# Performance work log

Measured on AMD Instinct MI355X. Metric: run time of the kernel, lower is better.

The kernel has to match this reference:

```python
import jax, jax.numpy as jnp
import numpy as np

E = 256      # feat_dim
H = 4        # num_heads
D = E // H   # head_dim = 64
NC = 7       # num_classes
B = 65536
EPS = 1e-5


def layernorm(x, g, b):
    mu = jnp.mean(x, axis=-1, keepdims=True)
    var = jnp.mean((x - mu) ** 2, axis=-1, keepdims=True)
    return (x - mu) * jax.lax.rsqrt(var + EPS) * g + b


def setup_inputs() -> dict:
    key = jax.random.key(0)
    ks = jax.random.split(key, 16)
    s = 0.02
    return {
        "f_swin":   jax.random.normal(ks[0], (B, E), jnp.float32),
        "f_maxvit": jax.random.normal(ks[1], (B, E), jnp.float32),
        "f_focal":  jax.random.normal(ks[2], (B, E), jnp.float32),
        # MultiheadAttention params (torch packs q,k,v into in_proj)
        "in_proj_w": jax.random.normal(ks[3], (3 * E, E), jnp.float32) * s,
        "in_proj_b": jnp.zeros((3 * E,), jnp.float32),
        "out_w": jax.random.normal(ks[4], (E, E), jnp.float32) * s,
        "out_b": jnp.zeros((E,), jnp.float32),
        # fusion LayerNorm
        "ln1_g": jnp.ones((E,), jnp.float32),
        "ln1_b": jnp.zeros((E,), jnp.float32),
        # gate: Linear(3E, 3)
        "gate_w": jax.random.normal(ks[5], (3, 3 * E), jnp.float32) * s,
        "gate_b": jnp.zeros((3,), jnp.float32),
        # deep_head: LN -> Linear(E,256) -> GELU -> Linear(256,128) -> GELU -> Linear(128,7)
        "ln2_g": jnp.ones((E,), jnp.float32),
        "ln2_b": jnp.zeros((E,), jnp.float32),
        "w1": jax.random.normal(ks[6], (256, E), jnp.float32) * s,
        "b1": jnp.zeros((256,), jnp.float32),
        "w2": jax.random.normal(ks[7], (128, 256), jnp.float32) * s,
        "b2": jnp.zeros((128,), jnp.float32),
        "w3": jax.random.normal(ks[8], (NC, 128), jnp.float32) * s,
        "b3": jnp.zeros((NC,), jnp.float32),
    }


def reference(f_swin, f_maxvit, f_focal, in_proj_w, in_proj_b, out_w, out_b,
              ln1_g, ln1_b, gate_w, gate_b, ln2_g, ln2_b,
              w1, b1, w2, b2, w3, b3):
    # --- AttentionFusionModule ---
    stacked = jnp.stack([f_swin, f_maxvit, f_focal], axis=1)  # [B,3,E]
    qkv = stacked @ in_proj_w.T + in_proj_b                   # [B,3,3E]
    q, k, v = jnp.split(qkv, 3, axis=-1)
    # [B,3,E] -> [B,H,3,D]
    def to_heads(t):
        return t.reshape(t.shape[0], 3, H, D).transpose(0, 2, 1, 3)
    qh, kh, vh = to_heads(q), to_heads(k), to_heads(v)
    scores = jnp.einsum('bhqd,bhkd->bhqk', qh, kh) / jnp.sqrt(jnp.float32(D))
    attn = jax.nn.softmax(scores, axis=-1)
    ctx = jnp.einsum('bhqk,bhkd->bhqd', attn, vh)             # [B,H,3,D]
    ctx = ctx.transpose(0, 2, 1, 3).reshape(-1, 3, E)         # [B,3,E]
    att_out = ctx @ out_w.T + out_b
    x = layernorm(att_out + stacked, ln1_g, ln1_b)            # [B,3,E]
    concat = jnp.concatenate([f_swin, f_maxvit, f_focal], axis=-1)  # [B,3E]
    weights = jax.nn.softmax(concat @ gate_w.T + gate_b, axis=-1)   # [B,3]
    fused = jnp.einsum('bse,bs->be', x, weights)              # [B,E]
    # --- deep_head (Dropout inactive at inference; exact GELU as in torch) ---
    h = layernorm(fused, ln2_g, ln2_b)
    h = jax.nn.gelu(h @ w1.T + b1, approximate=False)
    h = jax.nn.gelu(h @ w2.T + b2, approximate=False)
    logits = h @ w3.T + b3
    return logits, fused
```

## Files before the change

kernel.cpp:

```cpp
#include <hip/hip_runtime.h>
#include <math.h>


#define E   256
#define NC  7
#define BM  16
#define TOK 48
#define NT  256
#define BSX 264
#define BSB 136

typedef unsigned short u16;
typedef unsigned int   u32;
typedef __attribute__((ext_vector_type(8))) short  short8;
typedef __attribute__((ext_vector_type(4))) float  f32x4;

#define O_IPW 0
#define O_OW  196608
#define O_GW  262144
#define O_W1  264448
#define O_W2  329984
#define CVT_TOTAL 362752

__device__ __forceinline__ float bf2f(u32 u) { return __uint_as_float(u << 16); }
__device__ __forceinline__ u16 f2bf(float f) {
    u32 u = __float_as_uint(f);
    return (u16)((u + 0x7fffu + ((u >> 16) & 1u)) >> 16);
}

__global__ void cvt_weights(const float* __restrict__ ipw, const float* __restrict__ ow,
                            const float* __restrict__ gw,  const float* __restrict__ w1,
                            const float* __restrict__ w2,  u16* __restrict__ ws) {
    int i4 = (blockIdx.x * 256 + threadIdx.x) * 4;
    if (i4 >= CVT_TOTAL) return;
    const float* src; int off;
    if      (i4 < O_OW)  { src = ipw; off = i4; }
    else if (i4 < O_GW)  { src = ow;  off = i4 - O_OW; }
    else if (i4 < O_W1)  { src = gw;  off = i4 - O_GW; }
    else if (i4 < O_W2)  { src = w1;  off = i4 - O_W1; }
    else                 { src = w2;  off = i4 - O_W2; }
    float4 v = *(const float4*)(src + off);
    ushort4 o;
    o.x = f2bf(v.x); o.y = f2bf(v.y); o.z = f2bf(v.z); o.w = f2bf(v.w);
    *(ushort4*)(ws + i4) = o;
}

template<int MT, int NTW, int KSN, int AS, bool ZERO>
__device__ __forceinline__ void gemm_tile(const u16* aLds, int aRow0, int aCol0,
                                          const u16* __restrict__ bW, int rowBase, int bCol0,
                                          int lane, f32x4 (&acc)[MT][NTW]) {
    const int l16 = lane & 15, quad = lane >> 4;
    if (ZERO) {
        #pragma unroll
        for (int m = 0; m < MT; ++m)
            #pragma unroll
            for (int j = 0; j < NTW; ++j) acc[m][j] = (f32x4){0.f, 0.f, 0.f, 0.f};
    }
    #pragma unroll
    for (int ks = 0; ks < KSN; ++ks) {
        short8 a[MT];
        #pragma unroll
        for (int m = 0; m < MT; ++m)
            a[m] = *(const short8*)(aLds + (size_t)(aRow0 + m * 16 + l16) * AS + aCol0 + ks * 32 + quad * 8);
        #pragma unroll
        for (int j = 0; j < NTW; ++j) {
            short8 b = *(const short8*)(bW + (size_t)(rowBase + j * 16 + l16) * 256 + bCol0 + ks * 32 + quad * 8);
            #pragma unroll
            for (int m = 0; m < MT; ++m)
                acc[m][j] = __builtin_amdgcn_mfma_f32_16x16x32_bf16(a[m], b, acc[m][j], 0, 0, 0);
        }
    }
}

__global__ __launch_bounds__(NT, 2)
void dhc_mfma_kernel(
    const float* __restrict__ f0, const float* __restrict__ f1, const float* __restrict__ f2,
    const float* __restrict__ ipb, const float* __restrict__ ob,
    const float* __restrict__ ln1g, const float* __restrict__ ln1b,
    const float* __restrict__ gb,
    const float* __restrict__ ln2g, const float* __restrict__ ln2b,
    const float* __restrict__ b1, const float* __restrict__ b2,
    const float* __restrict__ w3, const float* __restrict__ b3,
    const u16* __restrict__ ws, float* __restrict__ d_out, int nrows)
{
    __shared__ __align__(16) u16 s_x[TOK * BSX];
    __shared__ __align__(16) u16 s_buf[TOK * BSB];
    __shared__ __align__(16) float s_small[640];
    #define S_ATTN(r,h,q) s_small[((r) * 4 + (h)) * 9 + (q)]

    const int tid  = threadIdx.x;
    const int wid  = tid >> 6, lane = tid & 63;
    const int l16  = lane & 15, quad = lane >> 4;
    const long long row0 = (long long)blockIdx.x * BM;
    const size_t fused_base = (size_t)nrows * NC;

    auto gp_slot = [&](int i) -> float* {
        return (float*)(s_x + (i >> 2) * BSX + 256) + (i & 3);
    };

    const u16* ipw_b = ws + O_IPW;
    const u16* ow_b  = ws + O_OW;
    const u16* gw_b  = ws + O_GW;
    const u16* w1_b  = ws + O_W1;
    const u16* w2_b  = ws + O_W2;

    #pragma unroll
    for (int it = 0; it < 12; ++it) {
        int id = it * NT + tid;
        int t  = id >> 6;
        int c4 = (id & 63) * 4;
        int s  = t >> 4, r = t & 15;
        float4 v = {0.f, 0.f, 0.f, 0.f};
        if (row0 + r < nrows) {
            const float* src = (s == 0 ? f0 : (s == 1 ? f1 : f2));
            v = *(const float4*)(src + (size_t)(row0 + r) * E + c4);
        }
        ushort4 o;
        o.x = f2bf(v.x); o.y = f2bf(v.y); o.z = f2bf(v.z); o.w = f2bf(v.w);
        *(ushort4*)(s_x + t * BSX + c4) = o;
    }
    __syncthreads();

    auto softmax_head = [&](int hh) {
        int i = tid >> 4, r = tid & 15;
        const u16* qrow = s_buf + (i * 16 + r) * BSB;
        const u16* k0 = s_buf + (0 * 16 + r) * BSB + 64;
        const u16* k1 = s_buf + (1 * 16 + r) * BSB + 64;
        const u16* k2 = s_buf + (2 * 16 + r) * BSB + 64;
        float d0a = 0.f, d0b = 0.f, d1a = 0.f, d1b = 0.f, d2a = 0.f, d2b = 0.f;
        #pragma unroll
        for (int d8 = 0; d8 < 8; ++d8) {
            short8 qv = *(const short8*)(qrow + d8 * 8);
            short8 a0 = *(const short8*)(k0 + d8 * 8);
            short8 a1 = *(const short8*)(k1 + d8 * 8);
            short8 a2 = *(const short8*)(k2 + d8 * 8);
            #pragma unroll
            for (int e = 0; e < 4; ++e) {
                float qa = bf2f((u32)(u16)qv[e]);
                float qb = bf2f((u32)(u16)qv[e + 4]);
                d0a += qa * bf2f((u32)(u16)a0[e]); d0b += qb * bf2f((u32)(u16)a0[e + 4]);
                d1a += qa * bf2f((u32)(u16)a1[e]); d1b += qb * bf2f((u32)(u16)a1[e + 4]);
                d2a += qa * bf2f((u32)(u16)a2[e]); d2b += qb * bf2f((u32)(u16)a2[e + 4]);
            }
        }
        float d0 = (d0a + d0b) * 0.125f, d1 = (d1a + d1b) * 0.125f, d2 = (d2a + d2b) * 0.125f;
        float mx = fmaxf(d0, fmaxf(d1, d2));
        float e0 = __expf(d0 - mx), e1 = __expf(d1 - mx), e2 = __expf(d2 - mx);
        float inv = 1.f / (e0 + e1 + e2);
        S_ATTN(r, hh, i * 3 + 0) = e0 * inv;
        S_ATTN(r, hh, i * 3 + 1) = e1 * inv;
        S_ATTN(r, hh, i * 3 + 2) = e2 * inv;
    };

    for (int h = 0; h < 4; ++h) {
        const int rbh = (wid < 2) ? (64 * h + 32 * wid)
                                  : (256 + 64 * h + 32 * (wid - 2));
        f32x4 acc[3][2];
        gemm_tile<3, 2, 8, BSX, true>(s_x, 0, 0, ipw_b, rbh, 0, lane, acc);
        if (h > 0 && tid < 48) softmax_head(h - 1);
        if (h == 0 && tid >= 48 && tid < 192) {
            int idx = tid - 48;
            int r = idx / 9, rem = idx % 9;
            int g = rem / 3, s = rem % 3;
            const u16* xp = s_x + (s * 16 + r) * BSX;
            const u16* wp = gw_b + g * 768 + s * 256;
            float a0 = 0.f, a1 = 0.f, a2 = 0.f, a3 = 0.f;
            for (int c8 = 0; c8 < 8; ++c8) {
                #pragma unroll
                for (int q4 = 0; q4 < 4; ++q4) {
                    short8 xv = *(const short8*)(xp + (c8 * 4 + q4) * 8);
                    short8 wv = *(const short8*)(wp + (c8 * 4 + q4) * 8);
                    float t = 0.f;
                    #pragma unroll
                    for (int e = 0; e < 8; ++e)
                        t += bf2f((u32)(u16)xv[e]) * bf2f((u32)(u16)wv[e]);
                    if      (q4 == 0) a0 += t;
                    else if (q4 == 1) a1 += t;
                    else if (q4 == 2) a2 += t;
                    else              a3 += t;
                }
            }
            *gp_slot(idx) = (a0 + a1) + (a2 + a3);
        }
        if (h == 1 && tid >= 48 && tid < 64) {
            int r = tid - 48;
            float l[3];
            #pragma unroll
            for (int g = 0; g < 3; ++g)
                l[g] = gb[g] + *gp_slot(r * 9 + g * 3 + 0)
                             + *gp_slot(r * 9 + g * 3 + 1)
                             + *gp_slot(r * 9 + g * 3 + 2);
            float mx = fmaxf(l[0], fmaxf(l[1], l[2]));
            float e0 = __expf(l[0] - mx), e1 = __expf(l[1] - mx), e2 = __expf(l[2] - mx);
            float inv = 1.f / (e0 + e1 + e2);
            s_small[576 + r * 3 + 0] = e0 * inv;
            s_small[576 + r * 3 + 1] = e1 * inv;
            s_small[576 + r * 3 + 2] = e2 * inv;
        }
        __syncthreads();
        const int nl = (wid < 2) ? (32 * wid) : (64 + 32 * (wid - 2));
        #pragma unroll
        for (int j = 0; j < 2; ++j) {
            int nn = nl + j * 16 + l16;
            float bias = ipb[rbh + j * 16 + l16];
            #pragma unroll
            for (int m = 0; m < 3; ++m)
                #pragma unroll
                for (int rr = 0; rr < 4; ++rr) {
                    int tok = m * 16 + quad * 4 + rr;
                    s_buf[tok * BSB + nn] = f2bf(acc[m][j][rr] + bias);
                }
        }
        __syncthreads();
    }

    f32x4 acc3[3][4];

    for (int hv = 0; hv < 2; ++hv) {
        {
            const int rb = 512 + 128 * hv + 32 * wid;
            f32x4 acc[3][2];
            gemm_tile<3, 2, 8, BSX, true>(s_x, 0, 0, ipw_b, rb, 0, lane, acc);
            if (hv == 0 && tid < 48) softmax_head(3);
            __syncthreads();
            #pragma unroll
            for (int j = 0; j < 2; ++j) {
                int nn = 32 * wid + j * 16 + l16;
                float bias = ipb[rb + j * 16 + l16];
                #pragma unroll
                for (int m = 0; m < 3; ++m)
                    #pragma unroll
                    for (int rr = 0; rr < 4; ++rr) {
                        int tok = m * 16 + quad * 4 + rr;
                        s_buf[tok * BSB + nn] = f2bf(acc[m][j][rr] + bias);
                    }
            }
        }
        __syncthreads();
        {
            int r  = tid >> 4;
            int cb = (tid & 15) * 8;
            int h  = 2 * hv + (cb >> 6);
            float a[9];
            #pragma unroll
            for (int q2 = 0; q2 < 9; ++q2) a[q2] = S_ATTN(r, h, q2);
            #pragma unroll
            for (int cc = 0; cc < 8; ++cc) {
                int c = cb + cc;
                float v0 = bf2f((u32)s_buf[(0 * 16 + r) * BSB + c]);
                float v1 = bf2f((u32)s_buf[(1 * 16 + r) * BSB + c]);
                float v2 = bf2f((u32)s_buf[(2 * 16 + r) * BSB + c]);
                float c0 = a[0] * v0 + a[1] * v1 + a[2] * v2;
                float c1 = a[3] * v0 + a[4] * v1 + a[5] * v2;
                float c2 = a[6] * v0 + a[7] * v1 + a[8] * v2;
                s_buf[(0 * 16 + r) * BSB + c] = f2bf(c0);
                s_buf[(1 * 16 + r) * BSB + c] = f2bf(c1);
                s_buf[(2 * 16 + r) * BSB + c] = f2bf(c2);
            }
        }
        __syncthreads();
        if (hv == 0) {
            gemm_tile<3, 4, 4, BSB, true >(s_buf, 0, 0, ow_b, 64 * wid, 0,   lane, acc3);
        } else {
            gemm_tile<3, 4, 4, BSB, false>(s_buf, 0, 0, ow_b, 64 * wid, 128, lane, acc3);
            #pragma unroll
            for (int j = 0; j < 4; ++j) {
                int n = 64 * wid + j * 16 + l16;
                float bias = ob[n];
                #pragma unroll
                for (int m = 0; m < 3; ++m)
                    #pragma unroll
                    for (int rr = 0; rr < 4; ++rr) {
                        int tok = m * 16 + quad * 4 + rr;
                        float v = acc3[m][j][rr] + bias + bf2f((u32)s_x[tok * BSX + n]);
                        s_x[tok * BSX + n] = f2bf(v);
                    }
            }
        }
        __syncthreads();
    }

    if (tid < 192) {
        int r = tid >> 2, j = tid & 3;
        const u16* xp = s_x + r * BSX + j * 64;
        float s0 = 0.f, s1 = 0.f, q0 = 0.f, q1 = 0.f;
        #pragma unroll
        for (int c8 = 0; c8 < 8; ++c8) {
            short8 v = *(const short8*)(xp + c8 * 8);
            #pragma unroll
            for (int e = 0; e < 4; ++e) {
                float xa = bf2f((u32)(u16)v[e]);
                float xb = bf2f((u32)(u16)v[e + 4]);
                s0 += xa; q0 += xa * xa;
                s1 += xb; q1 += xb * xb;
            }
        }
        float sum = s0 + s1, sq = q0 + q1;
        sum += __shfl_xor(sum, 1); sq += __shfl_xor(sq, 1);
        sum += __shfl_xor(sum, 2); sq += __shfl_xor(sq, 2);
        if (j == 0) {
            float mu = sum * (1.f / 256.f);
            float var = sq * (1.f / 256.f) - mu * mu;
            s_small[r] = mu;
            s_small[48 + r] = rsqrtf(var + 1e-5f);
        }
    }
    __syncthreads();
    {
        float g = ln1g[tid], b = ln1b[tid];
        #pragma unroll 4
        for (int t = 0; t < TOK; ++t) {
            float x = bf2f((u32)s_x[t * BSX + tid]);
            s_x[t * BSX + tid] = f2bf((x - s_small[t]) * s_small[48 + t] * g + b);
        }
    }
    __syncthreads();

    {
        int c = tid;
        float* outF = d_out + fused_base;
        #pragma unroll 4
        for (int r = 0; r < BM; ++r) {
            float w0 = s_small[576 + r * 3 + 0];
            float w1v = s_small[576 + r * 3 + 1];
            float w2v = s_small[576 + r * 3 + 2];
            float f = w0  * bf2f((u32)s_x[(0 * 16 + r) * BSX + c])
                    + w1v * bf2f((u32)s_x[(1 * 16 + r) * BSX + c])
                    + w2v * bf2f((u32)s_x[(2 * 16 + r) * BSX + c]);
            if (row0 + r < nrows) outF[(size_t)(row0 + r) * E + c] = f;
            s_buf[r * BSX + c] = f2bf(f);
        }
    }
    __syncthreads();

    {
        int r = tid >> 4, j = tid & 15;
        const u16* fp = s_buf + r * BSX + j * 16;
        float sum = 0.f, sq = 0.f;
        #pragma unroll
        for (int c8 = 0; c8 < 2; ++c8) {
            short8 v = *(const short8*)(fp + c8 * 8);
            #pragma unroll
            for (int e = 0; e < 8; ++e) {
                float x = bf2f((u32)(u16)v[e]);
                sum += x; sq += x * x;
            }
        }
        sum += __shfl_xor(sum, 1); sq += __shfl_xor(sq, 1);
        sum += __shfl_xor(sum, 2); sq += __shfl_xor(sq, 2);
        sum += __shfl_xor(sum, 4); sq += __shfl_xor(sq, 4);
        sum += __shfl_xor(sum, 8); sq += __shfl_xor(sq, 8);
        if (j == 0) {
            float mu = sum * (1.f / 256.f);
            float var = sq * (1.f / 256.f) - mu * mu;
            s_small[96 + r] = mu;
            s_small[112 + r] = rsqrtf(var + 1e-5f);
        }
    }
    __syncthreads();
    {
        float g = ln2g[tid], b = ln2b[tid];
        #pragma unroll
        for (int r = 0; r < BM; ++r) {
            float x = bf2f((u32)s_buf[r * BSX + tid]);
            s_buf[r * BSX + tid] = f2bf((x - s_small[96 + r]) * s_small[112 + r] * g + b);
        }
    }
    __syncthreads();

    {
        f32x4 acc[1][4];
        gemm_tile<1, 4, 8, BSX, true>(s_buf, 0, 0, w1_b, 64 * wid, 0, lane, acc);
        __syncthreads();
        #pragma unroll
        for (int j = 0; j < 4; ++j) {
            int n = 64 * wid + j * 16 + l16;
            float bias = b1[n];
            #pragma unroll
            for (int rr = 0; rr < 4; ++rr) {
                int r = quad * 4 + rr;
                float x = acc[0][j][rr] + bias;
                float hgelu = 0.5f * x * (1.f + erff(x * 0.70710678118654752f));
                s_buf[r * BSX + n] = f2bf(hgelu);
            }
        }
    }
    __syncthreads();

    {
        f32x4 acc[1][2];
        gemm_tile<1, 2, 8, BSX, true>(s_buf, 0, 0, w2_b, 32 * wid, 0, lane, acc);
        __syncthreads();
        #pragma unroll
        for (int j = 0; j < 2; ++j) {
            int n = 32 * wid + j * 16 + l16;
            float bias = b2[n];
            #pragma unroll
            for (int rr = 0; rr < 4; ++rr) {
                int r = quad * 4 + rr;
                float x = acc[0][j][rr] + bias;
                float hgelu = 0.5f * x * (1.f + erff(x * 0.70710678118654752f));
                s_buf[r * BSB + n] = f2bf(hgelu);
            }
        }
    }
    __syncthreads();

    if (tid < BM * NC) {
        int r = tid / NC, n = tid % NC;
        const float* wr = w3 + n * 128;
        const u16* hp = s_buf + r * BSB;
        float a0 = 0.f, a1 = 0.f, a2 = 0.f, a3 = 0.f;
        #pragma unroll
        for (int q8 = 0; q8 < 8; ++q8) {
            #pragma unroll
            for (int q4 = 0; q4 < 4; ++q4) {
                int k4 = q8 * 4 + q4;
                float4 w = *(const float4*)(wr + k4 * 4);
                float t = bf2f((u32)hp[k4 * 4 + 0]) * w.x
                        + bf2f((u32)hp[k4 * 4 + 1]) * w.y
                        + bf2f((u32)hp[k4 * 4 + 2]) * w.z
                        + bf2f((u32)hp[k4 * 4 + 3]) * w.w;
                if      (q4 == 0) a0 += t;
                else if (q4 == 1) a1 += t;
                else if (q4 == 2) a2 += t;
                else              a3 += t;
            }
        }
        float acc = b3[n] + (a0 + a1) + (a2 + a3);
        if (row0 + r < nrows) d_out[(size_t)(row0 + r) * NC + n] = acc;
    }
}

extern "C" void kernel_launch(void* const* d_in, const int* in_sizes, int n_in,
                              void* d_out, int out_size, void* d_ws, size_t ws_size,
                              hipStream_t stream) {
    (void)n_in; (void)ws_size; (void)out_size;
    const int nrows = in_sizes[0] / E;
    u16* ws = (u16*)d_ws;
    cvt_weights<<<(CVT_TOTAL / 4 + 255) / 256, 256, 0, stream>>>(
        (const float*)d_in[3], (const float*)d_in[5], (const float*)d_in[9],
        (const float*)d_in[13], (const float*)d_in[15], ws);
    const int nblocks = (nrows + BM - 1) / BM;
    dhc_mfma_kernel<<<nblocks, NT, 0, stream>>>(
        (const float*)d_in[0], (const float*)d_in[1], (const float*)d_in[2],
        (const float*)d_in[4], (const float*)d_in[6],
        (const float*)d_in[7], (const float*)d_in[8],
        (const float*)d_in[10],
        (const float*)d_in[11], (const float*)d_in[12],
        (const float*)d_in[14], (const float*)d_in[16],
        (const float*)d_in[17], (const float*)d_in[18],
        ws, (float*)d_out, nrows);
}
```

Measured before the change: 716.5 us.

## Make each wave process its own rows independently, eliminating block barriers

Restructures the kernel so each of the four waves owns four batch rows (twelve tokens) with private LDS slices, removing all __syncthreads between stages. GEMMs become single-16-row-tile MFMA loops over full weight width per wave, with token tiles padded to sixteen. This removes barrier stalls and cross-wave coordination but wastes MFMA rows on padding and multiplies per-row weight reads from global/L2.

```diff
diff --git a/kernel.cpp b/kernel.cpp
--- a/kernel.cpp
+++ b/kernel.cpp
@@ -5,7 +5,6 @@
 #define E   256
 #define NC  7
 #define BM  16
-#define TOK 48
 #define NT  256
 #define BSX 264
 #define BSB 136
@@ -45,29 +44,22 @@
     *(ushort4*)(ws + i4) = o;
 }
 
-template<int MT, int NTW, int KSN, int AS, bool ZERO>
-__device__ __forceinline__ void gemm_tile(const u16* aLds, int aRow0, int aCol0,
-                                          const u16* __restrict__ bW, int rowBase, int bCol0,
-                                          int lane, f32x4 (&acc)[MT][NTW]) {
+template<int NTW, int KSN, bool ZERO>
+__device__ __forceinline__ void gemm1(const u16* aBase, int aStride, 
+                                      const u16* __restrict__ bW, int rowBase, int bCol0,
+                                      int lane, f32x4 (&acc)[NTW]) {
     const int l16 = lane & 15, quad = lane >> 4;
     if (ZERO) {
         #pragma unroll
-        for (int m = 0; m < MT; ++m)
-            #pragma unroll
-            for (int j = 0; j < NTW; ++j) acc[m][j] = (f32x4){0.f, 0.f, 0.f, 0.f};
+        for (int j = 0; j < NTW; ++j) acc[j] = (f32x4){0.f, 0.f, 0.f, 0.f};
     }
     #pragma unroll
     for (int ks = 0; ks < KSN; ++ks) {
-        short8 a[MT];
-        #pragma unroll
-        for (int m = 0; m < MT; ++m)
-            a[m] = *(const short8*)(aLds + (size_t)(aRow0 + m * 16 + l16) * AS + aCol0 + ks * 32 + quad * 8);
+        short8 a = *(const short8*)(aBase + (size_t)l16 * aStride + ks * 32 + quad * 8);
         #pragma unroll
         for (int j = 0; j < NTW; ++j) {
             short8 b = *(const short8*)(bW + (size_t)(rowBase + j * 16 + l16) * 256 + bCol0 + ks * 32 + quad * 8);
-            #pragma unroll
-            for (int m = 0; m < MT; ++m)
-                acc[m][j] = __builtin_amdgcn_mfma_f32_16x16x32_bf16(a[m], b, acc[m][j], 0, 0, 0);
+            acc[j] = __builtin_amdgcn_mfma_f32_16x16x32_bf16(a, b, acc[j], 0, 0, 0);
         }
     }
 }
@@ -83,20 +75,19 @@
     const float* __restrict__ w3, const float* __restrict__ b3,
     const u16* __restrict__ ws, float* __restrict__ d_out, int nrows)
 {
-    __shared__ __align__(16) u16 s_x[TOK * BSX];
-    __shared__ __align__(16) u16 s_buf[TOK * BSB];
-    __shared__ __align__(16) float s_small[640];
-    #define S_ATTN(r,h,q) s_small[((r) * 4 + (h)) * 9 + (q)]
+    __shared__ __align__(16) u16 s_x[64 * BSX];
+    __shared__ __align__(16) u16 s_buf[64 * BSB];
+    __shared__ __align__(16) float s_small[4 * 192];
 
     const int tid  = threadIdx.x;
     const int wid  = tid >> 6, lane = tid & 63;
     const int l16  = lane & 15, quad = lane >> 4;
-    const long long row0 = (long long)blockIdx.x * BM;
+    const long long row0 = (long long)blockIdx.x * BM + wid * 4;
     const size_t fused_base = (size_t)nrows * NC;
 
-    auto gp_slot = [&](int i) -> float* {
-        return (float*)(s_x + (i >> 2) * BSX + 256) + (i & 3);
-    };
+    u16*   sx = s_x   + wid * 16 * BSX;
+    u16*   sb = s_buf + wid * 16 * BSB;
+    float* sm = s_small + wid * 192;
 
     const u16* ipw_b = ws + O_IPW;
     const u16* ow_b  = ws + O_OW;
@@ -105,184 +96,158 @@
     const u16* w2_b  = ws + O_W2;
 
     #pragma unroll
-    for (int it = 0; it < 12; ++it) {
-        int id = it * NT + tid;
-        int t  = id >> 6;
-        int c4 = (id & 63) * 4;
-        int s  = t >> 4, r = t & 15;
+    for (int t = 0; t < 12; ++t) {
+        int s = t >> 2, r = t & 3;
         float4 v = {0.f, 0.f, 0.f, 0.f};
         if (row0 + r < nrows) {
             const float* src = (s == 0 ? f0 : (s == 1 ? f1 : f2));
-            v = *(const float4*)(src + (size_t)(row0 + r) * E + c4);
+            v = *(const float4*)(src + (size_t)(row0 + r) * E + lane * 4);
         }
         ushort4 o;
         o.x = f2bf(v.x); o.y = f2bf(v.y); o.z = f2bf(v.z); o.w = f2bf(v.w);
-        *(ushort4*)(s_x + t * BSX + c4) = o;
-    }
-    __syncthreads();
-
-    auto softmax_head = [&](int hh) {
-        int i = tid >> 4, r = tid & 15;
-        const u16* qrow = s_buf + (i * 16 + r) * BSB;
-        const u16* k0 = s_buf + (0 * 16 + r) * BSB + 64;
-        const u16* k1 = s_buf + (1 * 16 + r) * BSB + 64;
-        const u16* k2 = s_buf + (2 * 16 + r) * BSB + 64;
-        float d0a = 0.f, d0b = 0.f, d1a = 0.f, d1b = 0.f, d2a = 0.f, d2b = 0.f;
-        #pragma unroll
-        for (int d8 = 0; d8 < 8; ++d8) {
-            short8 qv = *(const short8*)(qrow + d8 * 8);
-            short8 a0 = *(const short8*)(k0 + d8 * 8);
-            short8 a1 = *(const short8*)(k1 + d8 * 8);
-            short8 a2 = *(const short8*)(k2 + d8 * 8);
-            #pragma unroll
-            for (int e = 0; e < 4; ++e) {
-                float qa = bf2f((u32)(u16)qv[e]);
-                float qb = bf2f((u32)(u16)qv[e + 4]);
-                d0a += qa * bf2f((u32)(u16)a0[e]); d0b += qb * bf2f((u32)(u16)a0[e + 4]);
-                d1a += qa * bf2f((u32)(u16)a1[e]); d1b += qb * bf2f((u32)(u16)a1[e + 4]);
-                d2a += qa * bf2f((u32)(u16)a2[e]); d2b += qb * bf2f((u32)(u16)a2[e + 4]);
-            }
-        }
-        float d0 = (d0a + d0b) * 0.125f, d1 = (d1a + d1b) * 0.125f, d2 = (d2a + d2b) * 0.125f;
-        float mx = fmaxf(d0, fmaxf(d1, d2));
-        float e0 = __expf(d0 - mx), e1 = __expf(d1 - mx), e2 = __expf(d2 - mx);
-        float inv = 1.f / (e0 + e1 + e2);
-        S_ATTN(r, hh, i * 3 + 0) = e0 * inv;
-        S_ATTN(r, hh, i * 3 + 1) = e1 * inv;
-        S_ATTN(r, hh, i * 3 + 2) = e2 * inv;
-    };
+        *(ushort4*)(sx + t * BSX + lane * 4) = o;
+    }
+    {
+        ushort4 z = {0, 0, 0, 0};
+        #pragma unroll
+        for (int t = 12; t < 16; ++t) *(ushort4*)(sx + t * BSX + lane * 4) = z;
+    }
+
+    if (lane < 36) {
+        int r = lane / 9, rem = lane % 9, g = rem / 3, s = rem % 3;
+        const u16* xp = sx + (s * 4 + r) * BSX;
+        const u16* wp = gw_b + g * 768 + s * 256;
+        float a0 = 0.f, a1 = 0.f, a2 = 0.f, a3 = 0.f;
+        #pragma unroll
+        for (int c8 = 0; c8 < 8; ++c8) {
+            #pragma unroll
+            for (int q4 = 0; q4 < 4; ++q4) {
+                short8 xv = *(const short8*)(xp + (c8 * 4 + q4) * 8);
+                short8 wv = *(const short8*)(wp + (c8 * 4 + q4) * 8);
+                float t = 0.f;
+                #pragma unroll
+                for (int e = 0; e < 8; ++e)
+                    t += bf2f((u32)(u16)xv[e]) * bf2f((u32)(u16)wv[e]);
+                if      (q4 == 0) a0 += t;
+                else if (q4 == 1) a1 += t;
+                else if (q4 == 2) a2 += t;
+                else              a3 += t;
+            }
+        }
+        float part = (a0 + a1) + (a2 + a3);
+        int base = r * 9 + g * 3;
+        float tot = __shfl(part, base) + __shfl(part, base + 1) + __shfl(part, base + 2);
+        float logit = tot + gb[g];
+        int br = r * 9;
+        float l0 = __shfl(logit, br + 0);
+        float l1 = __shfl(logit, br + 3);
+        float l2 = __shfl(logit, br + 6);
+        float mx = fmaxf(l0, fmaxf(l1, l2));
+        float e0 = __expf(l0 - mx), e1 = __expf(l1 - mx), e2 = __expf(l2 - mx);
+        float w = __expf(logit - mx) / (e0 + e1 + e2);
+        if (s == 0) sm[144 + r * 3 + g] = w;
+    }
 
     for (int h = 0; h < 4; ++h) {
-        const int rbh = (wid < 2) ? (64 * h + 32 * wid)
-                                  : (256 + 64 * h + 32 * (wid - 2));
-        f32x4 acc[3][2];
-        gemm_tile<3, 2, 8, BSX, true>(s_x, 0, 0, ipw_b, rbh, 0, lane, acc);
-        if (h > 0 && tid < 48) softmax_head(h - 1);
-        if (h == 0 && tid >= 48 && tid < 192) {
-            int idx = tid - 48;
-            int r = idx / 9, rem = idx % 9;
-            int g = rem / 3, s = rem % 3;
-            const u16* xp = s_x + (s * 16 + r) * BSX;
-            const u16* wp = gw_b + g * 768 + s * 256;
-            float a0 = 0.f, a1 = 0.f, a2 = 0.f, a3 = 0.f;
-            for (int c8 = 0; c8 < 8; ++c8) {
+        f32x4 aq[4], ak[4];
+        gemm1<4, 8, true>(sx, BSX, ipw_b, 64 * h, 0, lane, aq);
+        gemm1<4, 8, true>(sx, BSX, ipw_b, 256 + 64 * h, 0, lane, ak);
+        #pragma unroll
+        for (int j = 0; j < 4; ++j) {
+            float bq_ = ipb[64 * h + j * 16 + l16];
+            float bk_ = ipb[256 + 64 * h + j * 16 + l16];
+            #pragma unroll
+            for (int rr = 0; rr < 4; ++rr) {
+                int tok = quad * 4 + rr;
+                sb[tok * BSB + j * 16 + l16]      = f2bf(aq[j][rr] + bq_);
+                sb[tok * BSB + 64 + j * 16 + l16] = f2bf(ak[j][rr] + bk_);
+            }
+        }
+        if (lane < 12) {
+            int r = lane / 3, i = lane % 3;
+            const u16* qrow = sb + (i * 4 + r) * BSB;
+            const u16* k0 = sb + (0 + r) * BSB + 64;
+            const u16* k1 = sb + (4 + r) * BSB + 64;
+            const u16* k2 = sb + (8 + r) * BSB + 64;
+            float d0a = 0.f, d0b = 0.f, d1a = 0.f, d1b = 0.f, d2a = 0.f, d2b = 0.f;
+            #pragma unroll
+            for (int d8 = 0; d8 < 8; ++d8) {
+                short8 qv = *(const short8*)(qrow + d8 * 8);
+                short8 a0 = *(const short8*)(k0 + d8 * 8);
+                short8 a1 = *(const short8*)(k1 + d8 * 8);
+                short8 a2 = *(const short8*)(k2 + d8 * 8);
                 #pragma unroll
-                for (int q4 = 0; q4 < 4; ++q4) {
-                    short8 xv = *(const short8*)(xp + (c8 * 4 + q4) * 8);
-                    short8 wv = *(const short8*)(wp + (c8 * 4 + q4) * 8);
-                    float t = 0.f;
-                    #pragma unroll
-                    for (int e = 0; e < 8; ++e)
-                        t += bf2f((u32)(u16)xv[e]) * bf2f((u32)(u16)wv[e]);
-                    if      (q4 == 0) a0 += t;
-                    else if (q4 == 1) a1 += t;
-                    else if (q4 == 2) a2 += t;
-                    else              a3 += t;
+                for (int e = 0; e < 4; ++e) {
+                    float qa = bf2f((u32)(u16)qv[e]);
+                    float qb = bf2f((u32)(u16)qv[e + 4]);
+                    d0a += qa * bf2f((u32)(u16)a0[e]); d0b += qb * bf2f((u32)(u16)a0[e + 4]);
+                    d1a += qa * bf2f((u32)(u16)a1[e]); d1b += qb * bf2f((u32)(u16)a1[e + 4]);
+                    d2a += qa * bf2f((u32)(u16)a2[e]); d2b += qb * bf2f((u32)(u16)a2[e + 4]);
                 }
             }
-            *gp_slot(idx) = (a0 + a1) + (a2 + a3);
-        }
-        if (h == 1 && tid >= 48 && tid < 64) {
-            int r = tid - 48;
-            float l[3];
-            #pragma unroll
-            for (int g = 0; g < 3; ++g)
-                l[g] = gb[g] + *gp_slot(r * 9 + g * 3 + 0)
-                             + *gp_slot(r * 9 + g * 3 + 1)
-                             + *gp_slot(r * 9 + g * 3 + 2);
-            float mx = fmaxf(l[0], fmaxf(l[1], l[2]));
-            float e0 = __expf(l[0] - mx), e1 = __expf(l[1] - mx), e2 = __expf(l[2] - mx);
+            float d0 = (d0a + d0b) * 0.125f, d1 = (d1a + d1b) * 0.125f, d2 = (d2a + d2b) * 0.125f;
+            float mx = fmaxf(d0, fmaxf(d1, d2));
+            float e0 = __expf(d0 - mx), e1 = __expf(d1 - mx), e2 = __expf(d2 - mx);
             float inv = 1.f / (e0 + e1 + e2);
-            s_small[576 + r * 3 + 0] = e0 * inv;
-            s_small[576 + r * 3 + 1] = e1 * inv;
-            s_small[576 + r * 3 + 2] = e2 * inv;
-        }
-        __syncthreads();
-        const int nl = (wid < 2) ? (32 * wid) : (64 + 32 * (wid - 2));
-        #pragma unroll
-        for (int j = 0; j < 2; ++j) {
-            int nn = nl + j * 16 + l16;
-            float bias = ipb[rbh + j * 16 + l16];
-            #pragma unroll
-            for (int m = 0; m < 3; ++m)
+            float* ap = sm + (r * 4 + h) * 9 + i * 3;
+            ap[0] = e0 * inv; ap[1] = e1 * inv; ap[2] = e2 * inv;
+        }
+    }
+
+    {
+        f32x4 a3[16];
+        #pragma unroll
+        for (int j = 0; j < 16; ++j) a3[j] = (f32x4){0.f, 0.f, 0.f, 0.f};
+        for (int hv = 0; hv < 2; ++hv) {
+            f32x4 av[8];
+            gemm1<8, 8, true>(sx, BSX, ipw_b, 512 + 128 * hv, 0, lane, av);
+            #pragma unroll
+            for (int j = 0; j < 8; ++j) {
+                float bias = ipb[512 + 128 * hv + j * 16 + l16];
                 #pragma unroll
                 for (int rr = 0; rr < 4; ++rr) {
-                    int tok = m * 16 + quad * 4 + rr;
-                    s_buf[tok * BSB + nn] = f2bf(acc[m][j][rr] + bias);
+                    int tok = quad * 4 + rr;
+                    sb[tok * BSB + j * 16 + l16] = f2bf(av[j][rr] + bias);
                 }
-        }
-        __syncthreads();
-    }
-
-    f32x4 acc3[3][4];
-
-    for (int hv = 0; hv < 2; ++hv) {
-        {
-            const int rb = 512 + 128 * hv + 32 * wid;
-            f32x4 acc[3][2];
-            gemm_tile<3, 2, 8, BSX, true>(s_x, 0, 0, ipw_b, rb, 0, lane, acc);
-            if (hv == 0 && tid < 48) softmax_head(3);
-            __syncthreads();
-            #pragma unroll
-            for (int j = 0; j < 2; ++j) {
-                int nn = 32 * wid + j * 16 + l16;
-                float bias = ipb[rb + j * 16 + l16];
+            }
+            {
+                int r = lane >> 4, cg = lane & 15;
+                int h = 2 * hv + (cg >> 3);
+                float a[9];
                 #pragma unroll
-                for (int m = 0; m < 3; ++m)
-                    #pragma unroll
-                    for (int rr = 0; rr < 4; ++rr) {
-                        int tok = m * 16 + quad * 4 + rr;
-                        s_buf[tok * BSB + nn] = f2bf(acc[m][j][rr] + bias);
-                    }
-            }
-        }
-        __syncthreads();
-        {
-            int r  = tid >> 4;
-            int cb = (tid & 15) * 8;
-            int h  = 2 * hv + (cb >> 6);
-            float a[9];
-            #pragma unroll
-            for (int q2 = 0; q2 < 9; ++q2) a[q2] = S_ATTN(r, h, q2);
-            #pragma unroll
-            for (int cc = 0; cc < 8; ++cc) {
-                int c = cb + cc;
-                float v0 = bf2f((u32)s_buf[(0 * 16 + r) * BSB + c]);
-                float v1 = bf2f((u32)s_buf[(1 * 16 + r) * BSB + c]);
-                float v2 = bf2f((u32)s_buf[(2 * 16 + r) * BSB + c]);
-                float c0 = a[0] * v0 + a[1] * v1 + a[2] * v2;
-                float c1 = a[3] * v0 + a[4] * v1 + a[5] * v2;
-                float c2 = a[6] * v0 + a[7] * v1 + a[8] * v2;
-                s_buf[(0 * 16 + r) * BSB + c] = f2bf(c0);
-                s_buf[(1 * 16 + r) * BSB + c] = f2bf(c1);
-                s_buf[(2 * 16 + r) * BSB + c] = f2bf(c2);
-            }
-        }
-        __syncthreads();
-        if (hv == 0) {
-            gemm_tile<3, 4, 4, BSB, true >(s_buf, 0, 0, ow_b, 64 * wid, 0,   lane, acc3);
-        } else {
-            gemm_tile<3, 4, 4, BSB, false>(s_buf, 0, 0, ow_b, 64 * wid, 128, lane, acc3);
-            #pragma unroll
-            for (int j = 0; j < 4; ++j) {
-                int n = 64 * wid + j * 16 + l16;
-                float bias = ob[n];
+                for (int q2 = 0; q2 < 9; ++q2) a[q2] = sm[(r * 4 + h) * 9 + q2];
                 #pragma unroll
-                for (int m = 0; m < 3; ++m)
-                    #pragma unroll
-                    for (int rr = 0; rr < 4; ++rr) {
-                        int tok = m * 16 + quad * 4 + rr;
-                        float v = acc3[m][j][rr] + bias + bf2f((u32)s_x[tok * BSX + n]);
-                        s_x[tok * BSX + n] = f2bf(v);
-                    }
-            }
-        }
-        __syncthreads();
-    }
-
-    if (tid < 192) {
-        int r = tid >> 2, j = tid & 3;
-        const u16* xp = s_x + r * BSX + j * 64;
+                for (int cc = 0; cc < 8; ++cc) {
+                    int c = cg * 8 + cc;
+                    float v0 = bf2f((u32)sb[(0 + r) * BSB + c]);
+                    float v1 = bf2f((u32)sb[(4 + r) * BSB + c]);
+                    float v2 = bf2f((u32)sb[(8 + r) * BSB + c]);
+                    float c0 = a[0] * v0 + a[1] * v1 + a[2] * v2;
+                    float c1 = a[3] * v0 + a[4] * v1 + a[5] * v2;
+                    float c2 = a[6] * v0 + a[7] * v1 + a[8] * v2;
+                    sb[(0 + r) * BSB + c] = f2bf(c0);
+                    sb[(4 + r) * BSB + c] = f2bf(c1);
+                    sb[(8 + r) * BSB + c] = f2bf(c2);
+                }
+            }
+            gemm1<16, 4, false>(sb, BSB, ow_b, 0, 128 * hv, lane, a3);
+        }
+        #pragma unroll
+        for (int j = 0; j < 16; ++j) {
+            int n = j * 16 + l16;
+            float bias = ob[n];
+            #pragma unroll
+            for (int rr = 0; rr < 4; ++rr) {
+                int tok = quad * 4 + rr;
+                float vv = a3[j][rr] + bias + bf2f((u32)sx[tok * BSX + n]);
+                sx[tok * BSX + n] = f2bf(vv);
+            }
+        }
+    }
+
+    if (lane < 48) {
+        int r12 = lane >> 2, jj = lane & 3;
+        const u16* xp = sx + r12 * BSX + jj * 64;
         float s0 = 0.f, s1 = 0.f, q0 = 0.f, q1 = 0.f;
         #pragma unroll
         for (int c8 = 0; c8 < 8; ++c8) {
@@ -298,44 +263,56 @@
         float sum = s0 + s1, sq = q0 + q1;
         sum += __shfl_xor(sum, 1); sq += __shfl_xor(sq, 1);
         sum += __shfl_xor(sum, 2); sq += __shfl_xor(sq, 2);
-        if (j == 0) {
+        if (jj == 0) {
             float mu = sum * (1.f / 256.f);
             float var = sq * (1.f / 256.f) - mu * mu;
-            s_small[r] = mu;
-            s_small[48 + r] = rsqrtf(var + 1e-5f);
-        }
-    }
-    __syncthreads();
-    {
-        float g = ln1g[tid], b = ln1b[tid];
-        #pragma unroll 4
-        for (int t = 0; t < TOK; ++t) {
-            float x = bf2f((u32)s_x[t * BSX + tid]);
-            s_x[t * BSX + tid] = f2bf((x - s_small[t]) * s_small[48 + t] * g + b);
-        }
-    }
-    __syncthreads();
-
-    {
-        int c = tid;
-        float* outF = d_out + fused_base;
-        #pragma unroll 4
-        for (int r = 0; r < BM; ++r) {
-            float w0 = s_small[576 + r * 3 + 0];
-            float w1v = s_small[576 + r * 3 + 1];
-            float w2v = s_small[576 + r * 3 + 2];
-            float f = w0  * bf2f((u32)s_x[(0 * 16 + r) * BSX + c])
-                    + w1v * bf2f((u32)s_x[(1 * 16 + r) * BSX + c])
-                    + w2v * bf2f((u32)s_x[(2 * 16 + r) * BSX + c]);
-            if (row0 + r < nrows) outF[(size_t)(row0 + r) * E + c] = f;
-            s_buf[r * BSX + c] = f2bf(f);
-        }
-    }
-    __syncthreads();
-
-    {
-        int r = tid >> 4, j = tid & 15;
-        const u16* fp = s_buf + r * BSX + j * 16;
+            sm[156 + r12] = mu;
+            sm[168 + r12] = rsqrtf(var + 1e-5f);
+        }
+    }
+    {
+        int c = lane * 4;
+        float4 gv = *(const float4*)(ln1g + c);
+        float4 bv = *(const float4*)(ln1b + c);
+        #pragma unroll
+        for (int t = 0; t < 12; ++t) {
+            float mu = sm[156 + t], rs = sm[168 + t];
+            ushort4 xv = *(ushort4*)(sx + t * BSX + c);
+            ushort4 o;
+            o.x = f2bf((bf2f(xv.x) - mu) * rs * gv.x + bv.x);
+            o.y = f2bf((bf2f(xv.y) - mu) * rs * gv.y + bv.y);
+            o.z = f2bf((bf2f(xv.z) - mu) * rs * gv.z + bv.z);
+            o.w = f2bf((bf2f(xv.w) - mu) * rs * gv.w + bv.w);
+            *(ushort4*)(sx + t * BSX + c) = o;
+        }
+    }
+
+    {
+        int c = lane * 4;
+        #pragma unroll
+        for (int r = 0; r < 4; ++r) {
+            float w0 = sm[144 + r * 3 + 0];
+            float w1v = sm[144 + r * 3 + 1];
+            float w2v = sm[144 + r * 3 + 2];
+            ushort4 x0 = *(ushort4*)(sx + (0 + r) * BSX + c);
+            ushort4 x1 = *(ushort4*)(sx + (4 + r) * BSX + c);
+            ushort4 x2 = *(ushort4*)(sx + (8 + r) * BSX + c);
+            float4 f;
+            f.x = w0 * bf2f(x0.x) + w1v * bf2f(x1.x) + w2v * bf2f(x2.x);
+            f.y = w0 * bf2f(x0.y) + w1v * bf2f(x1.y) + w2v * bf2f(x2.y);
+            f.z = w0 * bf2f(x0.z) + w1v * bf2f(x1.z) + w2v * bf2f(x2.z);
+            f.w = w0 * bf2f(x0.w) + w1v * bf2f(x1.w) + w2v * bf2f(x2.w);
+            if (row0 + r < nrows)
+                *(float4*)(d_out + fused_base + (size_t)(row0 + r) * E + c) = f;
+            ushort4 o;
+            o.x = f2bf(f.x); o.y = f2bf(f.y); o.z = f2bf(f.z); o.w = f2bf(f.w);
+            *(ushort4*)(sx + r * BSX + c) = o;
+        }
+    }
+
+    {
+        int r = lane >> 4, jj = lane & 15;
+        const u16* fp = sx + r * BSX + jj * 16;
         float sum = 0.f, sq = 0.f;
         #pragma unroll
         for (int c8 = 0; c8 < 2; ++c8) {
@@ -350,66 +327,68 @@
         sum += __shfl_xor(sum, 2); sq += __shfl_xor(sq, 2);
         sum += __shfl_xor(sum, 4); sq += __shfl_xor(sq, 4);
         sum += __shfl_xor(sum, 8); sq += __shfl_xor(sq, 8);
-        if (j == 0) {
+        if (jj == 0) {
             float mu = sum * (1.f / 256.f);
             float var = sq * (1.f / 256.f) - mu * mu;
-            s_small[96 + r] = mu;
-            s_small[112 + r] = rsqrtf(var + 1e-5f);
-        }
-    }
-    __syncthreads();
-    {
-        float g = ln2g[tid], b = ln2b[tid];
-        #pragma unroll
-        for (int r = 0; r < BM; ++r) {
-            float x = bf2f((u32)s_buf[r * BSX + tid]);
-            s_buf[r * BSX + tid] = f2bf((x - s_small[96 + r]) * s_small[112 + r] * g + b);
-        }
-    }
-    __syncthreads();
-
-    {
-        f32x4 acc[1][4];
-        gemm_tile<1, 4, 8, BSX, true>(s_buf, 0, 0, w1_b, 64 * wid, 0, lane, acc);
-        __syncthreads();
-        #pragma unroll
-        for (int j = 0; j < 4; ++j) {
-            int n = 64 * wid + j * 16 + l16;
+            sm[180 + r] = mu;
+            sm[184 + r] = rsqrtf(var + 1e-5f);
+        }
+    }
+    {
+        int c = lane * 4;
+        float4 gv = *(const float4*)(ln2g + c);
+        float4 bv = *(const float4*)(ln2b + c);
+        #pragma unroll
+        for (int r = 0; r < 4; ++r) {
+            float mu = sm[180 + r], rs = sm[184 + r];
+            ushort4 xv = *(ushort4*)(sx + r * BSX + c);
+            ushort4 o;
+            o.x = f2bf((bf2f(xv.x) - mu) * rs * gv.x + bv.x);
+            o.y = f2bf((bf2f(xv.y) - mu) * rs * gv.y + bv.y);
+            o.z = f2bf((bf2f(xv.z) - mu) * rs * gv.z + bv.z);
+            o.w = f2bf((bf2f(xv.w) - mu) * rs * gv.w + bv.w);
+            *(ushort4*)(sx + r * BSX + c) = o;
+        }
+    }
+
+    {
+        f32x4 a4[16];
+        gemm1<16, 8, true>(sx, BSX, w1_b, 0, 0, lane, a4);
+        #pragma unroll
+        for (int j = 0; j < 16; ++j) {
+            int n = j * 16 + l16;
             float bias = b1[n];
             #pragma unroll
             for (int rr = 0; rr < 4; ++rr) {
-                int r = quad * 4 + rr;
-                float x = acc[0][j][rr] + bias;
-                float hgelu = 0.5f * x * (1.f + erff(x * 0.70710678118654752f));
-                s_buf[r * BSX + n] = f2bf(hgelu);
-            }
-        }
-    }
-    __syncthreads();
-
-    {
-        f32x4 acc[1][2];
-        gemm_tile<1, 2, 8, BSX, true>(s_buf, 0, 0, w2_b, 32 * wid, 0, lane, acc);
-        __syncthreads();
-        #pragma unroll
-        for (int j = 0; j < 2; ++j) {
-            int n = 32 * wid + j * 16 + l16;
+                int tok = quad * 4 + rr;
+                float x = a4[j][rr] + bias;
+                float hg = 0.5f * x * (1.f + erff(x * 0.70710678118654752f));
+                sx[tok * BSX + n] = f2bf(hg);
+            }
+        }
+    }
+
+    {
+        f32x4 a5[8];
+        gemm1<8, 8, true>(sx, BSX, w2_b, 0, 0, lane, a5);
+        #pragma unroll
+        for (int j = 0; j < 8; ++j) {
+            int n = j * 16 + l16;
             float bias = b2[n];
             #pragma unroll
             for (int rr = 0; rr < 4; ++rr) {
-                int r = quad * 4 + rr;
-                float x = acc[0][j][rr] + bias;
-                float hgelu = 0.5f * x * (1.f + erff(x * 0.70710678118654752f));
-                s_buf[r * BSB + n] = f2bf(hgelu);
-            }
-        }
-    }
-    __syncthreads();
-
-    if (tid < BM * NC) {
-        int r = tid / NC, n = tid % NC;
+                int tok = quad * 4 + rr;
+                float x = a5[j][rr] + bias;
+                float hg = 0.5f * x * (1.f + erff(x * 0.70710678118654752f));
+                sb[tok * BSB + n] = f2bf(hg);
+            }
+        }
+    }
+
+    if (lane < 28) {
+        int r = lane / 7, n = lane % 7;
         const float* wr = w3 + n * 128;
-        const u16* hp = s_buf + r * BSB;
+        const u16* hp = sb + r * BSB;
         float a0 = 0.f, a1 = 0.f, a2 = 0.f, a3 = 0.f;
         #pragma unroll
         for (int q8 = 0; q8 < 8; ++q8) {
```

After: 1.852 ms. 2.59x slower.
